# Kernel optimization log

Measured on AMD Instinct MI355X. Metric: run time of the kernel, lower is better.

Reference implementation:

```python
import jax, jax.numpy as jnp
import numpy as np

D_TOTAL, H, D_HEAD, HID = 2048, 16, 128, 512
EPS = float(np.finfo(np.float32).eps)  # nn.RMSNorm eps=None -> dtype eps


def _xavier(key, shape):
    # xavier_uniform over last two dims (per-head init)
    fan_in, fan_out = shape[-2], shape[-1]
    limit = float(np.sqrt(6.0 / (fan_in + fan_out)))
    return jax.random.uniform(key, shape, jnp.float32, -limit, limit)


def setup_inputs() -> dict:
    key = jax.random.key(0)
    ks = jax.random.split(key, 6)
    x = jax.random.normal(ks[0], (4, 4096, D_TOTAL), jnp.float32)
    g = jnp.ones((D_TOTAL,), jnp.float32)  # RMSNorm weight
    w0 = _xavier(ks[1], (H, D_HEAD, HID))
    w1 = _xavier(ks[2], (H, HID, HID))
    w2 = _xavier(ks[3], (H, HID, HID))
    w3 = _xavier(ks[4], (H, HID, D_HEAD))
    return {"x": x, "g": g, "w0": w0, "w1": w1, "w2": w2, "w3": w3}


def _rms_norm(x, g):
    var = jnp.mean(jnp.square(x), axis=-1, keepdims=True)
    return x * jax.lax.rsqrt(var + EPS) * g


def reference(x, g, w0, w1, w2, w3):
    h = _rms_norm(x, g)
    lead = h.shape[:-1]
    hp = h.reshape(*lead, H, D_HEAD)  # (B,S,H,d_head)
    gelu = lambda t: jax.nn.gelu(t, approximate=False)
    hp = jnp.einsum('bshd,hde->bshe', hp, w0)
    hp = jnp.einsum('bshd,hde->bshe', gelu(hp), w1)
    hp = jnp.einsum('bshd,hde->bshe', gelu(hp), w2)
    hp = jnp.einsum('bshd,hde->bshe', gelu(hp), w3)
    return hp.reshape(*lead, D_TOTAL)
```

## Files before the change

kernel.cpp:

```cpp
#include <hip/hip_runtime.h>
#include <cstdint>
#include <cstddef>

#define N_TOK   16384
#define D_TOTAL 2048
#define N_HEAD  16
#define D_HEAD  128
#define HID     512
#define MT      64
#define RMS_EPS 1.1920929e-07f

typedef __attribute__((ext_vector_type(8)))  short  short8;
typedef __attribute__((ext_vector_type(4)))  float  float4_t;
typedef __attribute__((ext_vector_type(16))) float  f32x16;
typedef __attribute__((ext_vector_type(2)))  unsigned int uint2_t;

__device__ __forceinline__ unsigned short f2bf(float f) {
    union { float f; unsigned int i; } v; v.f = f;
    unsigned int b = v.i;
    b += 0x7FFFu + ((b >> 16) & 1u);
    return (unsigned short)(b >> 16);
}

__device__ __forceinline__ unsigned int cvt_pk_bf16(float lo, float hi) {
    unsigned int r;
    asm("v_cvt_pk_bf16_f32 %0, %1, %2" : "=v"(r) : "v"(lo), "v"(hi));
    return r;
}

__device__ __forceinline__ float fast_exp2(float x) {
#if __has_builtin(__builtin_amdgcn_exp2f)
    return __builtin_amdgcn_exp2f(x);
#else
    return exp2f(x);
#endif
}

__device__ __forceinline__ float gelu_exact(float x) {
    float ax = fabsf(x);
    float t  = __builtin_amdgcn_rcpf(fmaf(0.23164193f, ax, 1.0f));
    float poly = fmaf(fmaf(fmaf(fmaf(1.061405429f, t, -1.453152027f),
                               t, 1.421413741f), t, -0.284496736f),
                      t, 0.254829592f) * t;
    float e    = fast_exp2(x * x * -0.72134752f);
    float erfa = fmaf(-poly, e, 1.0f);
    return fmaf(0.5f * ax, erfa, 0.5f * x);
}

__global__ __launch_bounds__(256) void prep_kernel(
    const float* __restrict__ x, float* __restrict__ scale,
    const float* __restrict__ w0, const float* __restrict__ w1,
    const float* __restrict__ w2, const float* __restrict__ w3,
    const float* __restrict__ gw,
    unsigned short* __restrict__ wt0, unsigned short* __restrict__ wt1,
    unsigned short* __restrict__ wt2, unsigned short* __restrict__ wt3)
{
    int b = blockIdx.x;
    if (b < 4096) {
        const int lane  = threadIdx.x & 63;
        const int wv    = threadIdx.x >> 6;
        const int token = b * 4 + wv;
        const float* xp = x + (size_t)token * D_TOTAL;
        float s = 0.0f;
#pragma unroll
        for (int j = 0; j < 8; ++j) {
            float4 v = *(const float4*)(xp + (size_t)(j * 64 + lane) * 4);
            s += v.x * v.x + v.y * v.y + v.z * v.z + v.w * v.w;
        }
#pragma unroll
        for (int off = 32; off > 0; off >>= 1) s += __shfl_down(s, off, 64);
        if (lane == 0)
            scale[token] = rsqrtf(s * (1.0f / (float)D_TOTAL) + RMS_EPS);
        return;
    }

    b -= 4096;
    const float* in; unsigned short* out; int K, N; const float* gm = nullptr;
    if      (b <  256) { in = w0; out = wt0; K = 128; N = 512; gm = gw; }
    else if (b < 1280) { in = w1; out = wt1; K = 512; N = 512; b -= 256; }
    else if (b < 2304) { in = w2; out = wt2; K = 512; N = 512; b -= 1280; }
    else               { in = w3; out = wt3; K = 512; N = 128; b -= 2304; }

    const int ktiles = K >> 6, ntiles = N >> 6;
    const int h   = b / (ktiles * ntiles);
    const int rem = b % (ktiles * ntiles);
    const int kt  = rem / ntiles, nt = rem % ntiles;

    const float* src = in + (size_t)h * K * N + (size_t)(kt * 64) * N + nt * 64;
    unsigned short* dst = out + (size_t)h * N * K + (size_t)(nt * 64) * K + kt * 64;

    __shared__ unsigned short tile[64][72];

#pragma unroll
    for (int p = 0; p < 2; ++p) {
        int gi = threadIdx.x + p * 256;
        int r  = gi >> 3;
        int gc = (gi & 7) * 8;
        float mul = 1.0f;
        if (gm) mul = gm[(size_t)h * K + kt * 64 + r];
        float4 a  = *(const float4*)(src + (size_t)r * N + gc);
        float4 b4 = *(const float4*)(src + (size_t)r * N + gc + 4);
        unsigned short tmp[8];
        tmp[0]=f2bf(a.x*mul);  tmp[1]=f2bf(a.y*mul);  tmp[2]=f2bf(a.z*mul);  tmp[3]=f2bf(a.w*mul);
        tmp[4]=f2bf(b4.x*mul); tmp[5]=f2bf(b4.y*mul); tmp[6]=f2bf(b4.z*mul); tmp[7]=f2bf(b4.w*mul);
        *(uint4*)&tile[r][gc] = *(const uint4*)tmp;
    }
    __syncthreads();
#pragma unroll
    for (int p = 0; p < 2; ++p) {
        int gi  = threadIdx.x + p * 256;
        int r2  = gi >> 3;
        int gc2 = (gi & 7) * 8;
        unsigned short tmp[8];
#pragma unroll
        for (int j = 0; j < 8; ++j) tmp[j] = tile[gc2 + j][r2];
        *(uint4*)(dst + (size_t)r2 * K + gc2) = *(const uint4*)tmp;
    }
}

template<int K, int MTT, int NT>
__device__ __forceinline__ void stage_gemm32(
    const unsigned short* __restrict__ sA,
    const unsigned short* __restrict__ wt,
    int lane, int mt0, int nbase, f32x16 acc[MTT][NT])
{
#pragma unroll
    for (int mt = 0; mt < MTT; ++mt)
#pragma unroll
        for (int nt = 0; nt < NT; ++nt)
#pragma unroll
            for (int i = 0; i < 16; ++i) acc[mt][nt][i] = 0.0f;

    const int r31 = lane & 31;
    const int h   = lane >> 5;

    const char* arow[NT];
#pragma unroll
    for (int nt = 0; nt < NT; ++nt)
        arow[nt] = (const char*)(wt + (size_t)(nbase + nt * 32 + r31) * K + h * 8);

    const char* sab = (const char*)sA;
    unsigned int vb[MTT];
#pragma unroll
    for (int mt = 0; mt < MTT; ++mt) {
        unsigned int row = (unsigned)(mt0 + mt * 32 + r31);
        unsigned int r7  = row & 7u;
        unsigned int g0  = (r7 & 6u) | ((unsigned)h ^ (r7 & 1u));
        vb[mt] = row * 1024u + (g0 << 4);
    }

#pragma unroll
    for (int ks = 0; ks < K / 16; ++ks) {
        short8 a[NT], b[MTT];
#pragma unroll
        for (int nt = 0; nt < NT; ++nt)
            a[nt] = *(const short8*)(arow[nt] + ks * 32);
#pragma unroll
        for (int mt = 0; mt < MTT; ++mt)
            b[mt] = *(const short8*)(sab + (vb[mt] ^ (unsigned)(ks << 5)));
#pragma unroll
        for (int mt = 0; mt < MTT; ++mt)
#pragma unroll
            for (int nt = 0; nt < NT; ++nt)
                acc[mt][nt] = __builtin_amdgcn_mfma_f32_32x32x16_bf16(
                    a[nt], b[mt], acc[mt][nt], 0, 0, 0);
    }
}

template<int MTT, int NT>
__device__ __forceinline__ void epi_gelu32(
    unsigned short* __restrict__ sAct, int lane, int mt0, int nbase,
    f32x16 acc[MTT][NT])
{
    const int r31 = lane & 31;
    const int h   = lane >> 5;
#pragma unroll
    for (int mt = 0; mt < MTT; ++mt) {
        const int tok = mt0 + mt * 32 + r31;
        const unsigned int rbase = (unsigned)tok * HID;
        const int tk7 = tok & 7;
#pragma unroll
        for (int nt = 0; nt < NT; ++nt)
#pragma unroll
            for (int g = 0; g < 4; ++g) {
                const int col = nbase + nt * 32 + 8 * g + 4 * h;
                float g0 = gelu_exact(acc[mt][nt][4 * g + 0]);
                float g1 = gelu_exact(acc[mt][nt][4 * g + 1]);
                float g2 = gelu_exact(acc[mt][nt][4 * g + 2]);
                float g3 = gelu_exact(acc[mt][nt][4 * g + 3]);
                uint2_t v;
                v.x = cvt_pk_bf16(g0, g1);
                v.y = cvt_pk_bf16(g2, g3);
                const int gsw = (col >> 3) ^ tk7;
                *(uint2_t*)&sAct[rbase + gsw * 8 + (col & 7)] = v;
            }
    }
}

__global__ __launch_bounds__(512, 4) void fused_chain_kernel(
    const float*          __restrict__ x,
    const float*          __restrict__ scale,
    const unsigned short* __restrict__ wt0,
    const unsigned short* __restrict__ wt1,
    const unsigned short* __restrict__ wt2,
    const unsigned short* __restrict__ wt3,
    float*                __restrict__ out)
{
    __shared__ unsigned short sAct[MT * HID];

    const int tid  = threadIdx.x;
    const int lane = tid & 63;
    const int wv   = tid >> 6;
    const int bx    = blockIdx.x;
    const int xcd   = bx & 7;
    const int local = bx >> 3;
    const int head  = xcd * 2 + (local >> 8);
    const int tile  = local & 255;
    const int tok0  = tile * MT;

#pragma unroll
    for (int p = 0; p < 2; ++p) {
        int gi = tid + p * 512;
        int r  = gi >> 4;
        int gc = gi & 15;
        int token = tok0 + r;
        const float* xp = x + (size_t)token * D_TOTAL + head * D_HEAD + gc * 8;
        float4 xa = *(const float4*)(xp);
        float4 xb = *(const float4*)(xp + 4);
        float s = scale[token];
        unsigned int u[4];
        u[0] = cvt_pk_bf16(xa.x * s, xa.y * s);
        u[1] = cvt_pk_bf16(xa.z * s, xa.w * s);
        u[2] = cvt_pk_bf16(xb.x * s, xb.y * s);
        u[3] = cvt_pk_bf16(xb.z * s, xb.w * s);
        int gsw = gc ^ (r & 7);
        *(uint4*)&sAct[r * HID + gsw * 8] = *(const uint4*)u;
    }
    __syncthreads();

    f32x16 acc[2][2];
    const int nb = wv * 64;

    stage_gemm32<128, 2, 2>(sAct, wt0 + (size_t)head * HID * D_HEAD, lane, 0, nb, acc);
    __syncthreads();
    epi_gelu32<2, 2>(sAct, lane, 0, nb, acc);
    __syncthreads();

    stage_gemm32<512, 2, 2>(sAct, wt1 + (size_t)head * HID * HID, lane, 0, nb, acc);
    __syncthreads();
    epi_gelu32<2, 2>(sAct, lane, 0, nb, acc);
    __syncthreads();

    stage_gemm32<512, 2, 2>(sAct, wt2 + (size_t)head * HID * HID, lane, 0, nb, acc);
    __syncthreads();
    epi_gelu32<2, 2>(sAct, lane, 0, nb, acc);
    __syncthreads();

    const int mt4 = (wv >> 2) * 32;
    const int nt4 = (wv & 3) * 32;
    f32x16 acc2[1][1];
    stage_gemm32<512, 1, 1>(sAct, wt3 + (size_t)head * D_HEAD * HID, lane, mt4, nt4, acc2);

    const int r31 = lane & 31;
    const int h   = lane >> 5;
    const int token = tok0 + mt4 + r31;
#pragma unroll
    for (int g = 0; g < 4; ++g) {
        const int col = head * D_HEAD + nt4 + 8 * g + 4 * h;
        float4_t v;
        v[0] = acc2[0][0][4 * g + 0];
        v[1] = acc2[0][0][4 * g + 1];
        v[2] = acc2[0][0][4 * g + 2];
        v[3] = acc2[0][0][4 * g + 3];
        *(float4_t*)&out[(size_t)token * D_TOTAL + col] = v;
    }
}

extern "C" void kernel_launch(void* const* d_in, const int* in_sizes, int n_in,
                              void* d_out, int out_size, void* d_ws, size_t ws_size,
                              hipStream_t stream)
{
    const float* x  = (const float*)d_in[0];
    const float* gw = (const float*)d_in[1];
    const float* w0 = (const float*)d_in[2];
    const float* w1 = (const float*)d_in[3];
    const float* w2 = (const float*)d_in[4];
    const float* w3 = (const float*)d_in[5];
    float* out = (float*)d_out;

    float* scale = (float*)d_ws;
    unsigned short* wt0 = (unsigned short*)((char*)d_ws + 65536);
    unsigned short* wt1 = wt0 + (size_t)N_HEAD * HID * D_HEAD;
    unsigned short* wt2 = wt1 + (size_t)N_HEAD * HID * HID;
    unsigned short* wt3 = wt2 + (size_t)N_HEAD * HID * HID;

    prep_kernel<<<4096 + 2560, 256, 0, stream>>>(
        x, scale, w0, w1, w2, w3, gw, wt0, wt1, wt2, wt3);

    fused_chain_kernel<<<N_HEAD * (N_TOK / MT), 512, 0, stream>>>(
        x, scale, wt0, wt1, wt2, wt3, out);
}
```

Baseline: 933.6 us.

## Double token tile to 128 rows and software-prefetch weight fragments

Doubles the per-block token tile so each weight fragment loaded from global memory feeds twice as many MFMAs, and adds a two-deep register prefetch of the weight operand across k-steps. The goal is to cut weight traffic through L2 and hide global load latency. The activation buffer in LDS doubles, so fewer blocks fit per CU and latency hiding from occupancy drops.

```diff
diff --git a/kernel.cpp b/kernel.cpp
--- a/kernel.cpp
+++ b/kernel.cpp
@@ -7,7 +7,7 @@
 #define N_HEAD  16
 #define D_HEAD  128
 #define HID     512
-#define MT      64
+#define MT      128
 #define RMS_EPS 1.1920929e-07f
 
 typedef __attribute__((ext_vector_type(8)))  short  short8;
@@ -124,6 +124,7 @@
     const unsigned short* __restrict__ wt,
     int lane, int mt0, int nbase, f32x16 acc[MTT][NT])
 {
+    constexpr int NK = K / 16;
 #pragma unroll
     for (int mt = 0; mt < MTT; ++mt)
 #pragma unroll
@@ -149,12 +150,23 @@
         vb[mt] = row * 1024u + (g0 << 4);
     }
 
-#pragma unroll
-    for (int ks = 0; ks < K / 16; ++ks) {
-        short8 a[NT], b[MTT];
-#pragma unroll
-        for (int nt = 0; nt < NT; ++nt)
-            a[nt] = *(const short8*)(arow[nt] + ks * 32);
+    short8 apf[2][NT];
+#pragma unroll
+    for (int nt = 0; nt < NT; ++nt) apf[0][nt] = *(const short8*)(arow[nt]);
+#pragma unroll
+    for (int nt = 0; nt < NT; ++nt) apf[1][nt] = *(const short8*)(arow[nt] + 32);
+
+#pragma unroll
+    for (int ks = 0; ks < NK; ++ks) {
+        short8 a[NT];
+#pragma unroll
+        for (int nt = 0; nt < NT; ++nt) a[nt] = apf[ks & 1][nt];
+        if (ks + 2 < NK) {
+#pragma unroll
+            for (int nt = 0; nt < NT; ++nt)
+                apf[ks & 1][nt] = *(const short8*)(arow[nt] + (ks + 2) * 32);
+        }
+        short8 b[MTT];
 #pragma unroll
         for (int mt = 0; mt < MTT; ++mt)
             b[mt] = *(const short8*)(sab + (vb[mt] ^ (unsigned)(ks << 5)));
@@ -197,7 +209,7 @@
     }
 }
 
-__global__ __launch_bounds__(512, 4) void fused_chain_kernel(
+__global__ __launch_bounds__(512, 2) void fused_chain_kernel(
     const float*          __restrict__ x,
     const float*          __restrict__ scale,
     const unsigned short* __restrict__ wt0,
@@ -214,12 +226,12 @@
     const int bx    = blockIdx.x;
     const int xcd   = bx & 7;
     const int local = bx >> 3;
-    const int head  = xcd * 2 + (local >> 8);
-    const int tile  = local & 255;
+    const int head  = xcd * 2 + (local >> 7);
+    const int tile  = local & 127;
     const int tok0  = tile * MT;
 
 #pragma unroll
-    for (int p = 0; p < 2; ++p) {
+    for (int p = 0; p < 4; ++p) {
         int gi = tid + p * 512;
         int r  = gi >> 4;
         int gc = gi & 15;
@@ -238,41 +250,44 @@
     }
     __syncthreads();
 
-    f32x16 acc[2][2];
+    f32x16 acc[4][2];
     const int nb = wv * 64;
 
-    stage_gemm32<128, 2, 2>(sAct, wt0 + (size_t)head * HID * D_HEAD, lane, 0, nb, acc);
-    __syncthreads();
-    epi_gelu32<2, 2>(sAct, lane, 0, nb, acc);
-    __syncthreads();
-
-    stage_gemm32<512, 2, 2>(sAct, wt1 + (size_t)head * HID * HID, lane, 0, nb, acc);
-    __syncthreads();
-    epi_gelu32<2, 2>(sAct, lane, 0, nb, acc);
-    __syncthreads();
-
-    stage_gemm32<512, 2, 2>(sAct, wt2 + (size_t)head * HID * HID, lane, 0, nb, acc);
-    __syncthreads();
-    epi_gelu32<2, 2>(sAct, lane, 0, nb, acc);
-    __syncthreads();
-
-    const int mt4 = (wv >> 2) * 32;
+    stage_gemm32<128, 4, 2>(sAct, wt0 + (size_t)head * HID * D_HEAD, lane, 0, nb, acc);
+    __syncthreads();
+    epi_gelu32<4, 2>(sAct, lane, 0, nb, acc);
+    __syncthreads();
+
+    stage_gemm32<512, 4, 2>(sAct, wt1 + (size_t)head * HID * HID, lane, 0, nb, acc);
+    __syncthreads();
+    epi_gelu32<4, 2>(sAct, lane, 0, nb, acc);
+    __syncthreads();
+
+    stage_gemm32<512, 4, 2>(sAct, wt2 + (size_t)head * HID * HID, lane, 0, nb, acc);
+    __syncthreads();
+    epi_gelu32<4, 2>(sAct, lane, 0, nb, acc);
+    __syncthreads();
+
     const int nt4 = (wv & 3) * 32;
-    f32x16 acc2[1][1];
-    stage_gemm32<512, 1, 1>(sAct, wt3 + (size_t)head * D_HEAD * HID, lane, mt4, nt4, acc2);
+    const int mt4 = (wv >> 2) * 64;
+    f32x16 acc2[2][1];
+    stage_gemm32<512, 2, 1>(sAct, wt3 + (size_t)head * D_HEAD * HID, lane, mt4, nt4, acc2);
 
     const int r31 = lane & 31;
     const int h   = lane >> 5;
-    const int token = tok0 + mt4 + r31;
-#pragma unroll
-    for (int g = 0; g < 4; ++g) {
-        const int col = head * D_HEAD + nt4 + 8 * g + 4 * h;
-        float4_t v;
-        v[0] = acc2[0][0][4 * g + 0];
-        v[1] = acc2[0][0][4 * g + 1];
-        v[2] = acc2[0][0][4 * g + 2];
-        v[3] = acc2[0][0][4 * g + 3];
-        *(float4_t*)&out[(size_t)token * D_TOTAL + col] = v;
+#pragma unroll
+    for (int mt = 0; mt < 2; ++mt) {
+        const int token = tok0 + mt4 + mt * 32 + r31;
+#pragma unroll
+        for (int g = 0; g < 4; ++g) {
+            const int col = head * D_HEAD + nt4 + 8 * g + 4 * h;
+            float4_t v;
+            v[0] = acc2[mt][0][4 * g + 0];
+            v[1] = acc2[mt][0][4 * g + 1];
+            v[2] = acc2[mt][0][4 * g + 2];
+            v[3] = acc2[mt][0][4 * g + 3];
+            *(float4_t*)&out[(size_t)token * D_TOTAL + col] = v;
+        }
     }
 }
 
```

Result: faster. 824.9 us (-11.6%).
